# Kernel optimization log

Hardware: AMD Instinct MI355X
Metric: run time of the kernel (lower is better)

## Reference

```python
import jax, jax.numpy as jnp
import numpy as np
from jax import lax

T, B, H = 1024, 128, 512   # num_tokens, batch, encoder hidden
A, K, F = 128, 32, 31      # attention hidden, conv filters, filter length


def setup_inputs() -> dict:
    key = jax.random.key(0)
    ks = jax.random.split(key, 8)
    s = 0.05  # param init scale for numerical stability of tanh
    encoded_tokens = jax.random.normal(ks[0], (T, B, H), jnp.float32)
    query = jax.random.normal(ks[1], (B, H), jnp.float32)
    prev = jax.random.uniform(ks[2], (T, B), jnp.float32)
    previous_alignment = prev / jnp.sum(prev, axis=0, keepdims=True)  # prob-like alignment
    conv_filter = jax.random.normal(ks[3], (K, 1, F), jnp.float32) * s
    W_loc = jax.random.normal(ks[4], (K, A), jnp.float32) * s
    W_q = jax.random.normal(ks[5], (H, A), jnp.float32) * s
    W_k = jax.random.normal(ks[6], (H, A), jnp.float32) * s
    v = jax.random.normal(ks[7], (A,), jnp.float32) * s
    return {"encoded_tokens": encoded_tokens, "query": query,
            "previous_alignment": previous_alignment, "conv_filter": conv_filter,
            "W_loc": W_loc, "W_q": W_q, "W_k": W_k, "v": v}


def reference(encoded_tokens, query, previous_alignment, conv_filter, W_loc, W_q, W_k, v):
    pad = (conv_filter.shape[-1] - 1) // 2
    # Location features: conv1d over token axis of previous alignment.
    # previous_alignment [T,B] -> [B,1,T]; conv_filter [K,1,F] -> loc [B,K,T]
    loc = lax.conv_general_dilated(previous_alignment.T[:, None, :], conv_filter,
                                   window_strides=(1,), padding=[(pad, pad)],
                                   dimension_numbers=("NCH", "OIH", "NCH"))
    proc_loc = jnp.einsum("bkt,ka->tba", loc, W_loc)              # [T,B,A]
    proc_query = query @ W_q                                       # [B,A]
    proc_keys = jnp.einsum("tbh,ha->tba", encoded_tokens, W_k)    # [T,B,A]
    # Additive (Bahdanau) score with tanh nonlinearity.
    score = jnp.einsum("tba,a->tb", jnp.tanh(proc_keys + proc_loc + proc_query[None]), v)
    alignment = jax.nn.softmax(score, axis=0)                      # softmax over tokens [T,B]
    context = jnp.einsum("tb,tbh->bh", alignment, encoded_tokens)  # [B,H]
    return context, alignment
```

## Files before the change

kernel.cpp:

```cpp
#include <hip/hip_runtime.h>
#include <hip/hip_bf16.h>
#include <math.h>

#define T_DIM 1024
#define B_DIM 128
#define H_DIM 512
#define A_DIM 128
#define K_DIM 32
#define F_DIM 31

#define WS_WCOMB 0
#define WS_PQ    4096
#define WS_SCORE 20480
#define WS_PART  151552

#define KC 32

__global__ __launch_bounds__(256) void prep_kernel(
    const float* __restrict__ query, const float* __restrict__ conv_filter,
    const float* __restrict__ W_loc, const float* __restrict__ W_q,
    float* __restrict__ ws)
{
  int gid = blockIdx.x * 256 + threadIdx.x;
  if (blockIdx.x < 16) {
    if (gid < F_DIM * A_DIM) {
      int f = gid >> 7, a = gid & 127;
      float s = 0.f;
      #pragma unroll
      for (int k = 0; k < K_DIM; ++k)
        s += conv_filter[k * F_DIM + f] * W_loc[k * A_DIM + a];
      ws[WS_WCOMB + gid] = s;
    }
  } else {
    int idx = gid - 16 * 256;
    int b = idx >> 7, a = idx & 127;
    float s = 0.f;
    for (int h = 0; h < H_DIM; ++h)
      s += query[b * H_DIM + h] * W_q[h * A_DIM + a];
    ws[WS_PQ + idx] = s;
  }
}

__global__ __launch_bounds__(256, 2) void score_kernel(
    const float* __restrict__ enc, const float* __restrict__ wk,
    const float* __restrict__ prev, const float* __restrict__ ws,
    const float* __restrict__ vvec, float* __restrict__ score)
{
  __shared__ float encT[KC * 256];
  __shared__ float wkL[KC * 160];
  __shared__ float prevL[32 * 128];

  const int tid = threadIdx.x;
  const int t0 = blockIdx.x * 2;
  const int R0 = blockIdx.x * 256;
  const int rg = tid >> 3;
  const int cg = tid & 7;
  const int a0 = cg << 4;

  float acc[8][16];
  #pragma unroll
  for (int r = 0; r < 8; ++r)
    #pragma unroll
    for (int c = 0; c < 16; ++c) acc[r][c] = 0.f;

  #pragma unroll
  for (int it = 0; it < 4; ++it) {
    int seg = tid + it * 256;
    int rr = seg >> 5;
    int c4 = (seg & 31) << 2;
    int t = t0 - 15 + rr;
    float4 val = make_float4(0.f, 0.f, 0.f, 0.f);
    if (t >= 0 && t < T_DIM) val = *(const float4*)(prev + t * B_DIM + c4);
    *(float4*)(prevL + rr * 128 + c4) = val;
  }

  for (int hc = 0; hc < H_DIM; hc += KC) {
    __syncthreads();
    #pragma unroll
    for (int it = 0; it < 4; ++it) {
      int seg = tid + it * 256;
      int h = seg >> 5;
      int g = (seg >> 2) & 7;
      int w = (seg & 3) << 2;
      float4 val = *(const float4*)(wk + (hc + h) * A_DIM + g * 16 + w);
      *(float4*)(wkL + h * 160 + g * 20 + w) = val;
    }
    #pragma unroll
    for (int it = 0; it < 8; ++it) {
      int row = it * 32 + (tid >> 3);
      int j = tid & 7;
      float4 val = *(const float4*)(enc + (size_t)(R0 + row) * H_DIM + hc + (j << 2));
      int rsw = row ^ ((j & 3) << 3);
      encT[(j * 4 + 0) * 256 + rsw] = val.x;
      encT[(j * 4 + 1) * 256 + rsw] = val.y;
      encT[(j * 4 + 2) * 256 + rsw] = val.z;
      encT[(j * 4 + 3) * 256 + rsw] = val.w;
    }
    __syncthreads();
    #pragma unroll 4
    for (int h = 0; h < KC; ++h) {
      int q = (h >> 2) & 3;
      const float* wbase = wkL + h * 160 + cg * 20;
      float4 w0 = *(const float4*)(wbase);
      float4 w1 = *(const float4*)(wbase + 4);
      float4 w2 = *(const float4*)(wbase + 8);
      float4 w3 = *(const float4*)(wbase + 12);
      const float* ebase = encT + h * 256 + ((rg ^ q) << 3);
      float4 e0 = *(const float4*)(ebase);
      float4 e1 = *(const float4*)(ebase + 4);
      float wv[16] = {w0.x,w0.y,w0.z,w0.w, w1.x,w1.y,w1.z,w1.w,
                      w2.x,w2.y,w2.z,w2.w, w3.x,w3.y,w3.z,w3.w};
      float ev[8]  = {e0.x,e0.y,e0.z,e0.w, e1.x,e1.y,e1.z,e1.w};
      #pragma unroll
      for (int r = 0; r < 8; ++r)
        #pragma unroll
        for (int c = 0; c < 16; ++c)
          acc[r][c] = fmaf(ev[r], wv[c], acc[r][c]);
    }
  }

  #pragma unroll 1
  for (int f = 0; f < F_DIM; ++f) {
    const float* wc = ws + WS_WCOMB + f * A_DIM + a0;
    float4 c0 = *(const float4*)(wc);
    float4 c1 = *(const float4*)(wc + 4);
    float4 c2 = *(const float4*)(wc + 8);
    float4 c3 = *(const float4*)(wc + 12);
    float cv[16] = {c0.x,c0.y,c0.z,c0.w, c1.x,c1.y,c1.z,c1.w,
                    c2.x,c2.y,c2.z,c2.w, c3.x,c3.y,c3.z,c3.w};
    #pragma unroll
    for (int r = 0; r < 8; ++r) {
      int row = rg * 8 + r;
      float p = prevL[((row >> 7) + f) * 128 + (row & 127)];
      #pragma unroll
      for (int c = 0; c < 16; ++c) acc[r][c] = fmaf(p, cv[c], acc[r][c]);
    }
  }

  const float* vp = vvec + a0;
  float4 v0 = *(const float4*)(vp);
  float4 v1 = *(const float4*)(vp + 4);
  float4 v2 = *(const float4*)(vp + 8);
  float4 v3 = *(const float4*)(vp + 12);
  float vv[16] = {v0.x,v0.y,v0.z,v0.w, v1.x,v1.y,v1.z,v1.w,
                  v2.x,v2.y,v2.z,v2.w, v3.x,v3.y,v3.z,v3.w};
  float part[8];
  #pragma unroll
  for (int r = 0; r < 8; ++r) {
    int row = rg * 8 + r;
    int b = row & 127;
    const float* pqp = ws + WS_PQ + b * A_DIM + a0;
    float4 p0 = *(const float4*)(pqp);
    float4 p1 = *(const float4*)(pqp + 4);
    float4 p2 = *(const float4*)(pqp + 8);
    float4 p3 = *(const float4*)(pqp + 12);
    float pv[16] = {p0.x,p0.y,p0.z,p0.w, p1.x,p1.y,p1.z,p1.w,
                    p2.x,p2.y,p2.z,p2.w, p3.x,p3.y,p3.z,p3.w};
    float s = 0.f;
    #pragma unroll
    for (int c = 0; c < 16; ++c)
      s += tanhf(acc[r][c] + pv[c]) * vv[c];
    part[r] = s;
  }
  #pragma unroll
  for (int r = 0; r < 8; ++r) {
    float s = part[r];
    s += __shfl_xor(s, 1);
    s += __shfl_xor(s, 2);
    s += __shfl_xor(s, 4);
    if (cg == 0) {
      int row = rg * 8 + r;
      int b = row & 127;
      int t = t0 + (row >> 7);
      score[b * T_DIM + t] = s;
    }
  }
}

__global__ __launch_bounds__(256) void softmax_kernel(
    float* __restrict__ score, float* __restrict__ out_align)
{
  __shared__ float red[8];
  int b = blockIdx.x, tid = threadIdx.x;
  float v0[4];
  #pragma unroll
  for (int i = 0; i < 4; ++i) v0[i] = score[b * T_DIM + tid + i * 256];
  float m = fmaxf(fmaxf(v0[0], v0[1]), fmaxf(v0[2], v0[3]));
  #pragma unroll
  for (int off = 1; off < 64; off <<= 1) m = fmaxf(m, __shfl_xor(m, off));
  if ((tid & 63) == 0) red[tid >> 6] = m;
  __syncthreads();
  m = fmaxf(fmaxf(red[0], red[1]), fmaxf(red[2], red[3]));
  float s = 0.f;
  #pragma unroll
  for (int i = 0; i < 4; ++i) { v0[i] = expf(v0[i] - m); s += v0[i]; }
  #pragma unroll
  for (int off = 1; off < 64; off <<= 1) s += __shfl_xor(s, off);
  if ((tid & 63) == 0) red[4 + (tid >> 6)] = s;
  __syncthreads();
  float inv = 1.f / (red[4] + red[5] + red[6] + red[7]);
  #pragma unroll
  for (int i = 0; i < 4; ++i) {
    float a = v0[i] * inv;
    int t = tid + i * 256;
    score[b * T_DIM + t] = a;
    out_align[t * B_DIM + b] = a;
  }
}

__global__ __launch_bounds__(256) void context_partial(
    const float* __restrict__ enc, const float* __restrict__ align_bt,
    float* __restrict__ partial)
{
  int b  = blockIdx.x >> 3;
  int tc = blockIdx.x & 7;
  int tid = threadIdx.x;
  float2 acc = make_float2(0.f, 0.f);
  const float* ab = align_bt + b * T_DIM + tc * 128;
  const float* ebase = enc + ((size_t)(tc * 128) * B_DIM + b) * H_DIM + tid * 2;
  #pragma unroll 4
  for (int t = 0; t < 128; ++t) {
    float a = ab[t];
    float2 e = *(const float2*)(ebase + (size_t)t * B_DIM * H_DIM);
    acc.x += a * e.x;
    acc.y += a * e.y;
  }
  *(float2*)(partial + ((size_t)tc * B_DIM + b) * H_DIM + tid * 2) = acc;
}

__global__ __launch_bounds__(256) void context_reduce(
    const float* __restrict__ partial, float* __restrict__ ctx)
{
  int idx = blockIdx.x * 256 + threadIdx.x;
  float s = 0.f;
  #pragma unroll
  for (int tc = 0; tc < 8; ++tc) s += partial[tc * (B_DIM * H_DIM) + idx];
  ctx[idx] = s;
}

extern "C" void kernel_launch(void* const* d_in, const int* in_sizes, int n_in,
                              void* d_out, int out_size, void* d_ws, size_t ws_size,
                              hipStream_t stream)
{
  const float* enc   = (const float*)d_in[0];
  const float* query = (const float*)d_in[1];
  const float* prev  = (const float*)d_in[2];
  const float* filt  = (const float*)d_in[3];
  const float* wloc  = (const float*)d_in[4];
  const float* wq    = (const float*)d_in[5];
  const float* wkp   = (const float*)d_in[6];
  const float* vvec  = (const float*)d_in[7];
  float* out = (float*)d_out;
  float* ws  = (float*)d_ws;

  prep_kernel<<<80, 256, 0, stream>>>(query, filt, wloc, wq, ws);
  score_kernel<<<512, 256, 0, stream>>>(enc, wkp, prev, ws, vvec, ws + WS_SCORE);
  softmax_kernel<<<128, 256, 0, stream>>>(ws + WS_SCORE, out + B_DIM * H_DIM);
  context_partial<<<1024, 256, 0, stream>>>(enc, ws + WS_SCORE, ws + WS_PART);
  context_reduce<<<256, 256, 0, stream>>>(ws + WS_PART, out);
}
```

Baseline: 593.5 us.

## Move score GEMM and location conv to bf16x3 MFMA with split hi/lo operands

Replaces the scalar FP32 FMA GEMM in the score kernel with MFMA 32x32x16 bf16 instructions. Encoder activations and W_k are split into bf16 hi/lo pairs so three MFMAs recover near-FP32 accuracy. The location conv is folded in as a second small bf16 MFMA pass. The prep kernel now pre-splits and transposes W_k and the combined conv weights. It also uses a faster tanh, restructures the query projection, and unrolls the context_partial loop with four independent accumulators. The risk is reduced precision in the location term and the approximate tanh.

```diff
diff --git a/kernel.cpp b/kernel.cpp
--- a/kernel.cpp
+++ b/kernel.cpp
@@ -9,170 +9,236 @@
 #define K_DIM 32
 #define F_DIM 31
 
-#define WS_WCOMB 0
-#define WS_PQ    4096
-#define WS_SCORE 20480
-#define WS_PART  151552
-
-#define KC 32
+#define WS_PQ    0
+#define WS_SCORE 16384
+#define WS_WKHI  147456
+#define WS_WKLO  180224
+#define WS_WCT   212992
+#define WS_PART  147456
+
+typedef __attribute__((ext_vector_type(8)))  short bf16x8;
+typedef __attribute__((ext_vector_type(16))) float f32x16;
+
+__device__ __forceinline__ ushort f2bf(float x) {
+  unsigned u = __float_as_uint(x);
+  u += 0x7FFFu + ((u >> 16) & 1u);
+  return (ushort)(u >> 16);
+}
+__device__ __forceinline__ float bf2f(ushort h) {
+  return __uint_as_float(((unsigned)h) << 16);
+}
+__device__ __forceinline__ float fast_tanh(float x) {
+  float xc = fminf(10.f, fmaxf(-10.f, x));
+  float e2 = __expf(2.f * xc);
+  return __fdividef(e2 - 1.f, e2 + 1.f);
+}
 
 __global__ __launch_bounds__(256) void prep_kernel(
     const float* __restrict__ query, const float* __restrict__ conv_filter,
     const float* __restrict__ W_loc, const float* __restrict__ W_q,
-    float* __restrict__ ws)
-{
-  int gid = blockIdx.x * 256 + threadIdx.x;
-  if (blockIdx.x < 16) {
-    if (gid < F_DIM * A_DIM) {
-      int f = gid >> 7, a = gid & 127;
+    const float* __restrict__ W_k, float* __restrict__ ws)
+{
+  int blk = blockIdx.x, tid = threadIdx.x;
+  if (blk < 128) {
+    __shared__ float red[256];
+    int a = tid & 127, half = tid >> 7;
+    const float* q = query + blk * H_DIM + half * 256;
+    const float* w = W_q + (size_t)(half * 256) * A_DIM + a;
+    float s = 0.f;
+    #pragma unroll 8
+    for (int h = 0; h < 256; ++h) s = fmaf(q[h], w[(size_t)h * A_DIM], s);
+    red[tid] = s;
+    __syncthreads();
+    if (tid < 128) ws[WS_PQ + blk * A_DIM + tid] = red[tid] + red[tid + 128];
+  } else if (blk == 128) {
+    ushort* wct = (ushort*)(ws + WS_WCT);
+    for (int it = 0; it < 16; ++it) {
+      int e = tid + it * 256;
+      int f = e >> 7, a = e & 127;
       float s = 0.f;
-      #pragma unroll
-      for (int k = 0; k < K_DIM; ++k)
-        s += conv_filter[k * F_DIM + f] * W_loc[k * A_DIM + a];
-      ws[WS_WCOMB + gid] = s;
+      if (f < F_DIM) {
+        #pragma unroll
+        for (int k = 0; k < K_DIM; ++k)
+          s += conv_filter[k * F_DIM + f] * W_loc[k * A_DIM + a];
+      }
+      wct[a * 32 + f] = f2bf(s);
     }
   } else {
-    int idx = gid - 16 * 256;
-    int b = idx >> 7, a = idx & 127;
-    float s = 0.f;
-    for (int h = 0; h < H_DIM; ++h)
-      s += query[b * H_DIM + h] * W_q[h * A_DIM + a];
-    ws[WS_PQ + idx] = s;
+    ushort* wkhi = (ushort*)(ws + WS_WKHI);
+    ushort* wklo = (ushort*)(ws + WS_WKLO);
+    int h0 = (blk - 129) * 16;
+    int a = tid & 127, hh = tid >> 7;
+    #pragma unroll
+    for (int j = 0; j < 8; ++j) {
+      int h = h0 + hh * 8 + j;
+      float x = W_k[(size_t)h * A_DIM + a];
+      ushort hi = f2bf(x);
+      float lo = x - bf2f(hi);
+      wkhi[a * H_DIM + h] = hi;
+      wklo[a * H_DIM + h] = f2bf(lo);
+    }
   }
 }
 
 __global__ __launch_bounds__(256, 2) void score_kernel(
-    const float* __restrict__ enc, const float* __restrict__ wk,
-    const float* __restrict__ prev, const float* __restrict__ ws,
-    const float* __restrict__ vvec, float* __restrict__ score)
-{
-  __shared__ float encT[KC * 256];
-  __shared__ float wkL[KC * 160];
-  __shared__ float prevL[32 * 128];
+    const float* __restrict__ enc, const float* __restrict__ ws_f,
+    const float* __restrict__ prev, const float* __restrict__ vvec,
+    float* __restrict__ score)
+{
+  __shared__ ushort smA_hi[256 * 32];
+  __shared__ ushort smA_lo[256 * 32];
+  __shared__ ushort smB_hi[128 * 32];
+  __shared__ ushort smB_lo[128 * 32];
+  __shared__ float  prevL[32 * 128];
+
+  const ushort* wkhi = (const ushort*)(ws_f + WS_WKHI);
+  const ushort* wklo = (const ushort*)(ws_f + WS_WKLO);
+  const ushort* wct  = (const ushort*)(ws_f + WS_WCT);
+  const float*  pq   = ws_f + WS_PQ;
 
   const int tid = threadIdx.x;
   const int t0 = blockIdx.x * 2;
   const int R0 = blockIdx.x * 256;
-  const int rg = tid >> 3;
-  const int cg = tid & 7;
-  const int a0 = cg << 4;
-
-  float acc[8][16];
-  #pragma unroll
-  for (int r = 0; r < 8; ++r)
-    #pragma unroll
-    for (int c = 0; c < 16; ++c) acc[r][c] = 0.f;
+  const int lane = tid & 63, wv = tid >> 6;
+  const int l31 = lane & 31, g = lane >> 5;
+  const int wrow = wv * 64;
+
+  f32x16 acc[2][4];
+  #pragma unroll
+  for (int mf = 0; mf < 2; ++mf)
+    #pragma unroll
+    for (int nf = 0; nf < 4; ++nf)
+      acc[mf][nf] = (f32x16)(0.f);
 
   #pragma unroll
   for (int it = 0; it < 4; ++it) {
     int seg = tid + it * 256;
-    int rr = seg >> 5;
-    int c4 = (seg & 31) << 2;
+    int rr = seg >> 5, c4 = (seg & 31) << 2;
     int t = t0 - 15 + rr;
     float4 val = make_float4(0.f, 0.f, 0.f, 0.f);
     if (t >= 0 && t < T_DIM) val = *(const float4*)(prev + t * B_DIM + c4);
     *(float4*)(prevL + rr * 128 + c4) = val;
   }
 
-  for (int hc = 0; hc < H_DIM; hc += KC) {
+  for (int hc = 0; hc < H_DIM; hc += 32) {
     __syncthreads();
-    #pragma unroll
-    for (int it = 0; it < 4; ++it) {
-      int seg = tid + it * 256;
-      int h = seg >> 5;
-      int g = (seg >> 2) & 7;
-      int w = (seg & 3) << 2;
-      float4 val = *(const float4*)(wk + (hc + h) * A_DIM + g * 16 + w);
-      *(float4*)(wkL + h * 160 + g * 20 + w) = val;
-    }
     #pragma unroll
     for (int it = 0; it < 8; ++it) {
       int row = it * 32 + (tid >> 3);
-      int j = tid & 7;
-      float4 val = *(const float4*)(enc + (size_t)(R0 + row) * H_DIM + hc + (j << 2));
-      int rsw = row ^ ((j & 3) << 3);
-      encT[(j * 4 + 0) * 256 + rsw] = val.x;
-      encT[(j * 4 + 1) * 256 + rsw] = val.y;
-      encT[(j * 4 + 2) * 256 + rsw] = val.z;
-      encT[(j * 4 + 3) * 256 + rsw] = val.w;
+      int sub = tid & 7;
+      float4 v = *(const float4*)(enc + (size_t)(R0 + row) * H_DIM + hc + sub * 4);
+      ushort4 hi4, lo4;
+      hi4.x = f2bf(v.x); lo4.x = f2bf(v.x - bf2f(hi4.x));
+      hi4.y = f2bf(v.y); lo4.y = f2bf(v.y - bf2f(hi4.y));
+      hi4.z = f2bf(v.z); lo4.z = f2bf(v.z - bf2f(hi4.z));
+      hi4.w = f2bf(v.w); lo4.w = f2bf(v.w - bf2f(hi4.w));
+      int chunk = sub >> 1;
+      int boff = row * 64 + ((chunk ^ ((row >> 1) & 3)) << 4) + ((sub & 1) << 3);
+      *(ushort4*)((char*)smA_hi + boff) = hi4;
+      *(ushort4*)((char*)smA_lo + boff) = lo4;
+    }
+    #pragma unroll
+    for (int it = 0; it < 2; ++it) {
+      int a = it * 64 + (tid >> 2);
+      int q = tid & 3;
+      uint4 vh = *(const uint4*)(wkhi + (size_t)a * H_DIM + hc + q * 8);
+      uint4 vl = *(const uint4*)(wklo + (size_t)a * H_DIM + hc + q * 8);
+      int boff = a * 64 + ((q ^ ((a >> 1) & 3)) << 4);
+      *(uint4*)((char*)smB_hi + boff) = vh;
+      *(uint4*)((char*)smB_lo + boff) = vl;
     }
     __syncthreads();
-    #pragma unroll 4
-    for (int h = 0; h < KC; ++h) {
-      int q = (h >> 2) & 3;
-      const float* wbase = wkL + h * 160 + cg * 20;
-      float4 w0 = *(const float4*)(wbase);
-      float4 w1 = *(const float4*)(wbase + 4);
-      float4 w2 = *(const float4*)(wbase + 8);
-      float4 w3 = *(const float4*)(wbase + 12);
-      const float* ebase = encT + h * 256 + ((rg ^ q) << 3);
-      float4 e0 = *(const float4*)(ebase);
-      float4 e1 = *(const float4*)(ebase + 4);
-      float wv[16] = {w0.x,w0.y,w0.z,w0.w, w1.x,w1.y,w1.z,w1.w,
-                      w2.x,w2.y,w2.z,w2.w, w3.x,w3.y,w3.z,w3.w};
-      float ev[8]  = {e0.x,e0.y,e0.z,e0.w, e1.x,e1.y,e1.z,e1.w};
-      #pragma unroll
-      for (int r = 0; r < 8; ++r)
+    #pragma unroll
+    for (int kk = 0; kk < 2; ++kk) {
+      bf16x8 ah[2], al[2];
+      #pragma unroll
+      for (int mf = 0; mf < 2; ++mf) {
+        int row = wrow + mf * 32 + l31;
+        int boff = row * 64 + (((kk * 2 + g) ^ ((row >> 1) & 3)) << 4);
+        ah[mf] = *(const bf16x8*)((const char*)smA_hi + boff);
+        al[mf] = *(const bf16x8*)((const char*)smA_lo + boff);
+      }
+      #pragma unroll
+      for (int nf = 0; nf < 4; ++nf) {
+        int a = nf * 32 + l31;
+        int boff = a * 64 + (((kk * 2 + g) ^ ((a >> 1) & 3)) << 4);
+        bf16x8 bh = *(const bf16x8*)((const char*)smB_hi + boff);
+        bf16x8 bl = *(const bf16x8*)((const char*)smB_lo + boff);
         #pragma unroll
-        for (int c = 0; c < 16; ++c)
-          acc[r][c] = fmaf(ev[r], wv[c], acc[r][c]);
-    }
-  }
-
-  #pragma unroll 1
-  for (int f = 0; f < F_DIM; ++f) {
-    const float* wc = ws + WS_WCOMB + f * A_DIM + a0;
-    float4 c0 = *(const float4*)(wc);
-    float4 c1 = *(const float4*)(wc + 4);
-    float4 c2 = *(const float4*)(wc + 8);
-    float4 c3 = *(const float4*)(wc + 12);
-    float cv[16] = {c0.x,c0.y,c0.z,c0.w, c1.x,c1.y,c1.z,c1.w,
-                    c2.x,c2.y,c2.z,c2.w, c3.x,c3.y,c3.z,c3.w};
-    #pragma unroll
-    for (int r = 0; r < 8; ++r) {
-      int row = rg * 8 + r;
-      float p = prevL[((row >> 7) + f) * 128 + (row & 127)];
-      #pragma unroll
-      for (int c = 0; c < 16; ++c) acc[r][c] = fmaf(p, cv[c], acc[r][c]);
-    }
-  }
-
-  const float* vp = vvec + a0;
-  float4 v0 = *(const float4*)(vp);
-  float4 v1 = *(const float4*)(vp + 4);
-  float4 v2 = *(const float4*)(vp + 8);
-  float4 v3 = *(const float4*)(vp + 12);
-  float vv[16] = {v0.x,v0.y,v0.z,v0.w, v1.x,v1.y,v1.z,v1.w,
-                  v2.x,v2.y,v2.z,v2.w, v3.x,v3.y,v3.z,v3.w};
-  float part[8];
-  #pragma unroll
-  for (int r = 0; r < 8; ++r) {
-    int row = rg * 8 + r;
-    int b = row & 127;
-    const float* pqp = ws + WS_PQ + b * A_DIM + a0;
-    float4 p0 = *(const float4*)(pqp);
-    float4 p1 = *(const float4*)(pqp + 4);
-    float4 p2 = *(const float4*)(pqp + 8);
-    float4 p3 = *(const float4*)(pqp + 12);
-    float pv[16] = {p0.x,p0.y,p0.z,p0.w, p1.x,p1.y,p1.z,p1.w,
-                    p2.x,p2.y,p2.z,p2.w, p3.x,p3.y,p3.z,p3.w};
-    float s = 0.f;
-    #pragma unroll
-    for (int c = 0; c < 16; ++c)
-      s += tanhf(acc[r][c] + pv[c]) * vv[c];
-    part[r] = s;
-  }
-  #pragma unroll
-  for (int r = 0; r < 8; ++r) {
-    float s = part[r];
-    s += __shfl_xor(s, 1);
-    s += __shfl_xor(s, 2);
-    s += __shfl_xor(s, 4);
-    if (cg == 0) {
-      int row = rg * 8 + r;
+        for (int mf = 0; mf < 2; ++mf) {
+          acc[mf][nf] = __builtin_amdgcn_mfma_f32_32x32x16_bf16(ah[mf], bh, acc[mf][nf], 0, 0, 0);
+          acc[mf][nf] = __builtin_amdgcn_mfma_f32_32x32x16_bf16(ah[mf], bl, acc[mf][nf], 0, 0, 0);
+          acc[mf][nf] = __builtin_amdgcn_mfma_f32_32x32x16_bf16(al[mf], bh, acc[mf][nf], 0, 0, 0);
+        }
+      }
+    }
+  }
+
+  __syncthreads();
+  {
+    int trow = tid >> 7, bcol = tid & 127;
+    #pragma unroll
+    for (int q = 0; q < 4; ++q) {
+      bf16x8 pk;
+      #pragma unroll
+      for (int e = 0; e < 8; ++e) {
+        int f = q * 8 + e;
+        float pv = (f < F_DIM) ? prevL[(trow + f) * 128 + bcol] : 0.f;
+        pk[e] = (short)f2bf(pv);
+      }
+      int boff = tid * 64 + ((q ^ ((tid >> 1) & 3)) << 4);
+      *(bf16x8*)((char*)smA_hi + boff) = pk;
+    }
+    #pragma unroll
+    for (int it = 0; it < 2; ++it) {
+      int a = it * 64 + (tid >> 2);
+      int q = tid & 3;
+      uint4 vv = *(const uint4*)(wct + a * 32 + q * 8);
+      *(uint4*)((char*)smB_hi + a * 64 + ((q ^ ((a >> 1) & 3)) << 4)) = vv;
+    }
+  }
+  __syncthreads();
+  #pragma unroll
+  for (int kk = 0; kk < 2; ++kk) {
+    bf16x8 ah[2];
+    #pragma unroll
+    for (int mf = 0; mf < 2; ++mf) {
+      int row = wrow + mf * 32 + l31;
+      int boff = row * 64 + (((kk * 2 + g) ^ ((row >> 1) & 3)) << 4);
+      ah[mf] = *(const bf16x8*)((const char*)smA_hi + boff);
+    }
+    #pragma unroll
+    for (int nf = 0; nf < 4; ++nf) {
+      int a = nf * 32 + l31;
+      int boff = a * 64 + (((kk * 2 + g) ^ ((a >> 1) & 3)) << 4);
+      bf16x8 bh = *(const bf16x8*)((const char*)smB_hi + boff);
+      #pragma unroll
+      for (int mf = 0; mf < 2; ++mf)
+        acc[mf][nf] = __builtin_amdgcn_mfma_f32_32x32x16_bf16(ah[mf], bh, acc[mf][nf], 0, 0, 0);
+    }
+  }
+
+  float vval[4];
+  #pragma unroll
+  for (int nf = 0; nf < 4; ++nf) vval[nf] = vvec[nf * 32 + l31];
+  #pragma unroll
+  for (int mf = 0; mf < 2; ++mf) {
+    #pragma unroll
+    for (int reg = 0; reg < 16; ++reg) {
+      int row = wrow + mf * 32 + (reg & 3) + 8 * (reg >> 2) + 4 * g;
       int b = row & 127;
-      int t = t0 + (row >> 7);
-      score[b * T_DIM + t] = s;
+      float s = 0.f;
+      #pragma unroll
+      for (int nf = 0; nf < 4; ++nf) {
+        float u = acc[mf][nf][reg] + pq[b * A_DIM + nf * 32 + l31];
+        s = fmaf(fast_tanh(u), vval[nf], s);
+      }
+      s += __shfl_xor(s, 1); s += __shfl_xor(s, 2); s += __shfl_xor(s, 4);
+      s += __shfl_xor(s, 8); s += __shfl_xor(s, 16);
+      if (l31 == 0) {
+        int t = t0 + (row >> 7);
+        score[b * T_DIM + t] = s;
+      }
     }
   }
 }
@@ -215,17 +281,25 @@
   int b  = blockIdx.x >> 3;
   int tc = blockIdx.x & 7;
   int tid = threadIdx.x;
-  float2 acc = make_float2(0.f, 0.f);
   const float* ab = align_bt + b * T_DIM + tc * 128;
-  const float* ebase = enc + ((size_t)(tc * 128) * B_DIM + b) * H_DIM + tid * 2;
-  #pragma unroll 4
-  for (int t = 0; t < 128; ++t) {
-    float a = ab[t];
-    float2 e = *(const float2*)(ebase + (size_t)t * B_DIM * H_DIM);
-    acc.x += a * e.x;
-    acc.y += a * e.y;
-  }
-  *(float2*)(partial + ((size_t)tc * B_DIM + b) * H_DIM + tid * 2) = acc;
+  const float* eb = enc + ((size_t)(tc * 128) * B_DIM + b) * H_DIM + tid * 2;
+  const size_t stride = (size_t)B_DIM * H_DIM;
+  float2 a0 = {0.f, 0.f}, a1 = {0.f, 0.f}, a2 = {0.f, 0.f}, a3 = {0.f, 0.f};
+  for (int t = 0; t < 128; t += 4) {
+    float4 av = *(const float4*)(ab + t);
+    float2 e0 = *(const float2*)(eb + (size_t)(t + 0) * stride);
+    float2 e1 = *(const float2*)(eb + (size_t)(t + 1) * stride);
+    float2 e2 = *(const float2*)(eb + (size_t)(t + 2) * stride);
+    float2 e3 = *(const float2*)(eb + (size_t)(t + 3) * stride);
+    a0.x = fmaf(av.x, e0.x, a0.x); a0.y = fmaf(av.x, e0.y, a0.y);
+    a1.x = fmaf(av.y, e1.x, a1.x); a1.y = fmaf(av.y, e1.y, a1.y);
+    a2.x = fmaf(av.z, e2.x, a2.x); a2.y = fmaf(av.z, e2.y, a2.y);
+    a3.x = fmaf(av.w, e3.x, a3.x); a3.y = fmaf(av.w, e3.y, a3.y);
+  }
+  float2 r;
+  r.x = (a0.x + a1.x) + (a2.x + a3.x);
+  r.y = (a0.y + a1.y) + (a2.y + a3.y);
+  *(float2*)(partial + ((size_t)tc * B_DIM + b) * H_DIM + tid * 2) = r;
 }
 
 __global__ __launch_bounds__(256) void context_reduce(
@@ -253,8 +327,8 @@
   float* out = (float*)d_out;
   float* ws  = (float*)d_ws;
 
-  prep_kernel<<<80, 256, 0, stream>>>(query, filt, wloc, wq, ws);
-  score_kernel<<<512, 256, 0, stream>>>(enc, wkp, prev, ws, vvec, ws + WS_SCORE);
+  prep_kernel<<<161, 256, 0, stream>>>(query, filt, wloc, wq, wkp, ws);
+  score_kernel<<<512, 256, 0, stream>>>(enc, ws, prev, vvec, ws + WS_SCORE);
   softmax_kernel<<<128, 256, 0, stream>>>(ws + WS_SCORE, out + B_DIM * H_DIM);
   context_partial<<<1024, 256, 0, stream>>>(enc, ws + WS_SCORE, ws + WS_PART);
   context_reduce<<<256, 256, 0, stream>>>(ws + WS_PART, out);
```

Result: faster. 522.9 us (-11.9%).
